# Optimization experiments

Measured on AMD Instinct MI355X. Metric: run time of the kernel, lower is better.

Reference implementation:

```python
import jax, jax.numpy as jnp
import numpy as np

OUT_F, IN_F = 4096, 4096
N_FREQ = 10000
SCALING = 150.0


def iwht(x):
    """Unnormalized fast Walsh-Hadamard transform along axis 0. x: [n, m], n power of 2."""
    n, m = x.shape
    steps = int(np.log2(n))
    x = x.reshape((2,) * steps + (m,))
    for ax in range(steps):  # log2(n) butterfly stages
        a, b = jnp.split(x, 2, axis=ax)
        x = jnp.concatenate([a + b, a - b], axis=ax)
    return x.reshape(n, m)


def setup_inputs() -> dict:
    key = jax.random.key(0)
    k1, k2, k3, k4 = jax.random.split(key, 4)
    x = jax.random.normal(k1, (2, 512, IN_F), dtype=jnp.float32)
    weight = jax.random.normal(k2, (OUT_F, IN_F), dtype=jnp.float32) * 0.02
    spectrum = jax.random.normal(k3, (N_FREQ,), dtype=jnp.float32)
    indices = jax.random.randint(k4, (2, N_FREQ), 0, OUT_F, dtype=jnp.int64)
    return {"x": x, "weight": weight, "spectrum": spectrum, "indices": indices}


def reference(x, weight, spectrum, indices):
    out_f, in_f = weight.shape
    # sparse scatter of spectrum into dense (out, in) matrix
    dense = jnp.zeros((out_f, in_f), dtype=spectrum.dtype).at[indices[0], indices[1]].set(spectrum)
    # inverse WHT along out axis, scaled
    delta_w = iwht(dense) * (SCALING / np.sqrt(np.float32(out_f)))
    # F.linear(x, base_w + delta_w)
    return jnp.einsum('bsi,oi->bso', x, weight + delta_w.astype(x.dtype))
```

## Files before the change

### kernel.cpp

```cpp
#include <hip/hip_runtime.h>

typedef unsigned short ushort_t;

#define M_DIM 1024
#define N_DIM 4096
#define K_DIM 4096
#define NFREQ 10000
constexpr float SCALE = 150.0f / 64.0f;

typedef __bf16 bf16x8_t  __attribute__((ext_vector_type(8)));
typedef float  f32x16_t  __attribute__((ext_vector_type(16)));

__device__ inline ushort_t f2bf(float f) {
  union { float f; unsigned u; } v; v.f = f;
  unsigned r = v.u + 0x7fffu + ((v.u >> 16) & 1u);
  return (ushort_t)(r >> 16);
}

__global__ __launch_bounds__(256) void build_w4(
    const float* __restrict__ weight,
    const float* __restrict__ spectrum,
    const int* __restrict__ idx,
    const float* __restrict__ x,
    ushort_t* __restrict__ wb,
    ushort_t* __restrict__ xb) {
  if (blockIdx.y == 16) {
    int flat = blockIdx.x * 256 + threadIdx.x;
#pragma unroll 4
    for (int k = 0; k < 64; ++k) {
      int i = flat + k * 16384;
      float4 v = ((const float4*)x)[i];
      ushort4 o;
      o.x = f2bf(v.x); o.y = f2bf(v.y); o.z = f2bf(v.z); o.w = f2bf(v.w);
      ((ushort4*)xb)[i] = o;
    }
    return;
  }

  constexpr int CAP = 1024;
  __shared__ unsigned e_raw[CAP];
  __shared__ float    v_raw[CAP];
  __shared__ uint2    ev_srt[CAP];
  __shared__ int cnt;
  __shared__ int cstart[65];
  __shared__ int coff[64];
  __shared__ int ccnt[64];
  __shared__ unsigned walsh16[16];

  const int tid = threadIdx.x;
  const int ci0 = blockIdx.x * 64;
  const int o0  = blockIdx.y * 256;

  if (tid == 0) cnt = 0;
  if (tid < 64) ccnt[tid] = 0;
  if (tid < 16) {
    unsigned m = tid;
    unsigned w = (m & 1 ? 0xAAAAu : 0u) ^ (m & 2 ? 0xCCCCu : 0u)
               ^ (m & 4 ? 0xF0F0u : 0u) ^ (m & 8 ? 0xFF00u : 0u);
    walsh16[m] = w;
  }
  __syncthreads();

  for (int j = tid; j < NFREQ; j += 256) {
    int c = idx[NFREQ + j];
    if ((c >> 6) == (int)blockIdx.x) {
      int p = atomicAdd(&cnt, 1);
      if (p < CAP) {
        e_raw[p] = ((unsigned)(c & 63) << 26) | ((unsigned)j << 12) | (unsigned)idx[j];
        v_raw[p] = spectrum[j];
        atomicAdd(&ccnt[c & 63], 1);
      }
    }
  }
  __syncthreads();
  const int n = cnt < CAP ? cnt : CAP;

  if (tid < 64) {
    int v = ccnt[tid];
    int s = v;
    for (int d = 1; d < 64; d <<= 1) {
      int o = __shfl_up(s, d, 64);
      if (tid >= d) s += o;
    }
    cstart[tid + 1] = s;
    if (tid == 0) cstart[0] = 0;
    coff[tid] = s - v;
  }
  __syncthreads();
  for (int e = tid; e < n; e += 256) {
    unsigned w = e_raw[e];
    int dc = w >> 26;
    int p = atomicAdd(&coff[dc], 1);
    ev_srt[p] = make_uint2(w, __float_as_uint(v_raw[e]));
  }
  __syncthreads();

  for (int e = tid; e < n; e += 256) {
    uint2 ev = ev_srt[e];
    int dc = ev.x >> 26;
    unsigned r = ev.x & 0xFFFu, j = (ev.x >> 12) & 0x3FFFu;
    int s0 = cstart[dc], e0 = cstart[dc + 1];
    bool dead = false;
    for (int p = s0; p < e0; ++p) {
      unsigned w2 = ev_srt[p].x;
      if ((w2 & 0xFFFu) == r && ((w2 >> 12) & 0x3FFFu) > j) dead = true;
    }
    if (dead) ev_srt[e].y = 0u;
  }
  __syncthreads();

  const int dc0   = (tid & 15) * 4;
  const int rof   = tid >> 4;
  const int obase = o0 + rof * 16;

  float acc[4][16];
#pragma unroll
  for (int c = 0; c < 4; ++c)
#pragma unroll
    for (int j = 0; j < 16; ++j) acc[c][j] = 0.0f;

#pragma unroll
  for (int c = 0; c < 4; ++c) {
    const int s = cstart[dc0 + c], e = cstart[dc0 + c + 1];
    for (int p = s; p < e; ++p) {
      uint2 ev = ev_srt[p];
      unsigned r = ev.x & 0xFFFu;
      unsigned W = walsh16[r & 15u];
      unsigned sx = ev.y ^ ((unsigned)(__popc(obase & r) & 1) << 31);
#pragma unroll
      for (int j = 0; j < 16; ++j) {
        acc[c][j] += __uint_as_float(sx ^ ((W << (31 - j)) & 0x80000000u));
      }
    }
  }

  size_t g = (size_t)obase * K_DIM + ci0 + dc0;
#pragma unroll
  for (int j = 0; j < 16; ++j) {
    float4 w4 = *(const float4*)&weight[g];
    ushort4 ov;
    ov.x = f2bf(w4.x + SCALE * acc[0][j]);
    ov.y = f2bf(w4.y + SCALE * acc[1][j]);
    ov.z = f2bf(w4.z + SCALE * acc[2][j]);
    ov.w = f2bf(w4.w + SCALE * acc[3][j]);
    *(ushort4*)&wb[g] = ov;
    g += K_DIM;
  }
}

__global__ __launch_bounds__(256) void gemm_bt(
    const ushort_t* __restrict__ A,
    const ushort_t* __restrict__ B,
    float* __restrict__ C0,
    float* __restrict__ C1,
    int klen) {
  constexpr int BM = 128, BN = 128, BK = 64;
  __shared__ __align__(16) ushort_t As[BM * BK];
  __shared__ __align__(16) ushort_t Bs[BN * BK];

  const int tid  = threadIdx.x;
  const int wave = tid >> 6, lane = tid & 63;
  const int wrow = wave >> 1, wcol = wave & 1;
  const int l32  = lane & 31, half = lane >> 5;
  const int bm = blockIdx.y * BM, bn = blockIdx.x * BN;
  const int kbeg = blockIdx.z * klen;
  float* __restrict__ dst = blockIdx.z == 0
      ? C0 : C1 + (size_t)(blockIdx.z - 1) * M_DIM * N_DIM;

  const int srow8 = lane >> 3;
  const int sq    = lane & 7;

  f32x16_t acc[2][2] = {};

  for (int kt = kbeg; kt < kbeg + klen; kt += BK) {
#pragma unroll
    for (int c = 0; c < 4; ++c) {
      int ch = wave * 4 + c;
      int gr = ch * 8 + srow8;
      int qg = sq ^ (gr & 7);
      const ushort_t* ga = A + (size_t)(bm + gr) * K_DIM + kt + qg * 8;
      __builtin_amdgcn_global_load_lds(
          (const __attribute__((address_space(1))) void*)ga,
          (__attribute__((address_space(3))) void*)&As[ch * 512], 16, 0, 0);
      const ushort_t* gb = B + (size_t)(bn + gr) * K_DIM + kt + qg * 8;
      __builtin_amdgcn_global_load_lds(
          (const __attribute__((address_space(1))) void*)gb,
          (__attribute__((address_space(3))) void*)&Bs[ch * 512], 16, 0, 0);
    }
    __syncthreads();

    bf16x8_t af[2][4], bfr[2][4];
#pragma unroll
    for (int mi = 0; mi < 2; ++mi) {
#pragma unroll
      for (int h = 0; h < 4; ++h) {
        int q = h * 2 + half;
        int ar = wrow * 64 + mi * 32 + l32;
        af[mi][h]  = *(const bf16x8_t*)&As[ar * BK + ((q ^ (ar & 7)) * 8)];
        int br = wcol * 64 + mi * 32 + l32;
        bfr[mi][h] = *(const bf16x8_t*)&Bs[br * BK + ((q ^ (br & 7)) * 8)];
      }
    }
#pragma unroll
    for (int h = 0; h < 4; ++h)
#pragma unroll
      for (int mi = 0; mi < 2; ++mi)
#pragma unroll
        for (int nj = 0; nj < 2; ++nj)
          acc[mi][nj] = __builtin_amdgcn_mfma_f32_32x32x16_bf16(
              af[mi][h], bfr[nj][h], acc[mi][nj], 0, 0, 0);
    __syncthreads();
  }

#pragma unroll
  for (int mi = 0; mi < 2; ++mi) {
#pragma unroll
    for (int nj = 0; nj < 2; ++nj) {
      int col  = bn + wcol * 64 + nj * 32 + l32;
      int rwb  = bm + wrow * 64 + mi * 32 + 4 * half;
#pragma unroll
      for (int reg = 0; reg < 16; ++reg) {
        int row = rwb + (reg & 3) + 8 * (reg >> 2);
        dst[(size_t)row * N_DIM + col] = acc[mi][nj][reg];
      }
    }
  }
}

__global__ __launch_bounds__(256) void reduce_n(float* __restrict__ out,
                                                const float* __restrict__ part,
                                                int npart) {
  int i = blockIdx.x * 256 + threadIdx.x;
  float4 a = ((const float4*)out)[i];
  for (int t = 0; t < npart; ++t) {
    float4 b = ((const float4*)(part + (size_t)t * M_DIM * N_DIM))[i];
    a.x += b.x; a.y += b.y; a.z += b.z; a.w += b.w;
  }
  ((float4*)out)[i] = a;
}

extern "C" void kernel_launch(void* const* d_in, const int* in_sizes, int n_in,
                              void* d_out, int out_size, void* d_ws, size_t ws_size,
                              hipStream_t stream) {
  const float* x        = (const float*)d_in[0];
  const float* weight   = (const float*)d_in[1];
  const float* spectrum = (const float*)d_in[2];
  const int*   indices  = (const int*)d_in[3];
  float* out = (float*)d_out;

  char* ws = (char*)d_ws;
  const size_t WB_BYTES = (size_t)N_DIM * K_DIM * 2;
  const size_t XB_BYTES = (size_t)M_DIM * K_DIM * 2;
  const size_t P1_BYTES = (size_t)M_DIM * N_DIM * 4;

  ushort_t* wb = (ushort_t*)ws;
  ushort_t* xb = (ushort_t*)(ws + WB_BYTES);
  float* part = (float*)(ws + WB_BYTES + XB_BYTES);

  int zsplit = (ws_size >= WB_BYTES + XB_BYTES + P1_BYTES) ? 2 : 1;

  build_w4<<<dim3(64, 17), 256, 0, stream>>>(weight, spectrum, indices, x, wb, xb);

  gemm_bt<<<dim3(N_DIM / 128, M_DIM / 128, zsplit), 256, 0, stream>>>(
      xb, wb, out, part, K_DIM / zsplit);
  if (zsplit > 1)
    reduce_n<<<(M_DIM * N_DIM / 4) / 256, 256, 0, stream>>>(out, part, zsplit - 1);
}
```

Measured before the change: 185.5 us.

## Hoist sparse entry sorting into prep kernel and allow 4-way split-K

The per-column-group gather, counting sort and duplicate resolution of the sparse spectrum entries moves out of the weight-build kernel into a separate 64-block prep kernel. Its results are written to workspace, so each of the 16 row blocks per column group only loads them instead of redoing the 10000-index scan. The scratch area for these entries aliases the split-K partial buffer, which the GEMM only writes after the build kernel has consumed the entries. The GEMM split-K factor also rises to 4 when the workspace allows it. That gives more blocks in flight, but the final reduction must read three partial buffers and the launch sequence gains one extra kernel.

```diff
diff --git a/kernel.cpp b/kernel.cpp
--- a/kernel.cpp
+++ b/kernel.cpp
@@ -17,11 +17,84 @@
   return (ushort_t)(r >> 16);
 }
 
-__global__ __launch_bounds__(256) void build_w4(
-    const float* __restrict__ weight,
+__global__ __launch_bounds__(256) void prep_entries(
     const float* __restrict__ spectrum,
     const int* __restrict__ idx,
+    uint2* __restrict__ ent,
+    int* __restrict__ cst) {
+  constexpr int CAP = 1024;
+  __shared__ unsigned e_raw[CAP];
+  __shared__ float    v_raw[CAP];
+  __shared__ uint2    ev_srt[CAP];
+  __shared__ int cnt;
+  __shared__ int cstart[65];
+  __shared__ int coff[64];
+  __shared__ int ccnt[64];
+
+  const int tid = threadIdx.x;
+  const int g = blockIdx.x;
+
+  if (tid == 0) cnt = 0;
+  if (tid < 64) ccnt[tid] = 0;
+  __syncthreads();
+
+  for (int j = tid; j < NFREQ; j += 256) {
+    int c = idx[NFREQ + j];
+    if ((c >> 6) == g) {
+      int p = atomicAdd(&cnt, 1);
+      if (p < CAP) {
+        e_raw[p] = ((unsigned)(c & 63) << 26) | ((unsigned)j << 12) | (unsigned)idx[j];
+        v_raw[p] = spectrum[j];
+        atomicAdd(&ccnt[c & 63], 1);
+      }
+    }
+  }
+  __syncthreads();
+  const int n = cnt < CAP ? cnt : CAP;
+
+  if (tid < 64) {
+    int v = ccnt[tid];
+    int s = v;
+    for (int d = 1; d < 64; d <<= 1) {
+      int o = __shfl_up(s, d, 64);
+      if (tid >= d) s += o;
+    }
+    cstart[tid + 1] = s;
+    if (tid == 0) cstart[0] = 0;
+    coff[tid] = s - v;
+  }
+  __syncthreads();
+  for (int e = tid; e < n; e += 256) {
+    unsigned w = e_raw[e];
+    int dc = w >> 26;
+    int p = atomicAdd(&coff[dc], 1);
+    ev_srt[p] = make_uint2(w, __float_as_uint(v_raw[e]));
+  }
+  __syncthreads();
+
+  for (int e = tid; e < n; e += 256) {
+    uint2 ev = ev_srt[e];
+    int dc = ev.x >> 26;
+    unsigned r = ev.x & 0xFFFu, j = (ev.x >> 12) & 0x3FFFu;
+    int s0 = cstart[dc], e0 = cstart[dc + 1];
+    bool dead = false;
+    for (int p = s0; p < e0; ++p) {
+      unsigned w2 = ev_srt[p].x;
+      if ((w2 & 0xFFFu) == r && ((w2 >> 12) & 0x3FFFu) > j) dead = true;
+    }
+    if (dead) ev_srt[e].y = 0u;
+  }
+  __syncthreads();
+
+  for (int e = tid; e < n; e += 256) ent[g * CAP + e] = ev_srt[e];
+  if (tid < 65) cst[g * 72 + tid] = cstart[tid];
+}
+
+__global__ __launch_bounds__(256) void apply_w(
+    const float* __restrict__ weight,
     const float* __restrict__ x,
+    const uint2* __restrict__ ent,
+    const int* __restrict__ cst,
     ushort_t* __restrict__ wb,
     ushort_t* __restrict__ xb) {
   if (blockIdx.y == 16) {
@@ -38,75 +111,24 @@
   }
 
   constexpr int CAP = 1024;
-  __shared__ unsigned e_raw[CAP];
-  __shared__ float    v_raw[CAP];
-  __shared__ uint2    ev_srt[CAP];
-  __shared__ int cnt;
+  __shared__ uint2 ev[CAP];
   __shared__ int cstart[65];
-  __shared__ int coff[64];
-  __shared__ int ccnt[64];
   __shared__ unsigned walsh16[16];
 
   const int tid = threadIdx.x;
-  const int ci0 = blockIdx.x * 64;
+  const int g   = blockIdx.x;
+  const int ci0 = g * 64;
   const int o0  = blockIdx.y * 256;
 
-  if (tid == 0) cnt = 0;
-  if (tid < 64) ccnt[tid] = 0;
+  const int n = cst[g * 72 + 64];
+  if (tid < 65) cstart[tid] = cst[g * 72 + tid];
   if (tid < 16) {
     unsigned m = tid;
     unsigned w = (m & 1 ? 0xAAAAu : 0u) ^ (m & 2 ? 0xCCCCu : 0u)
                ^ (m & 4 ? 0xF0F0u : 0u) ^ (m & 8 ? 0xFF00u : 0u);
     walsh16[m] = w;
   }
-  __syncthreads();
-
-  for (int j = tid; j < NFREQ; j += 256) {
-    int c = idx[NFREQ + j];
-    if ((c >> 6) == (int)blockIdx.x) {
-      int p = atomicAdd(&cnt, 1);
-      if (p < CAP) {
-        e_raw[p] = ((unsigned)(c & 63) << 26) | ((unsigned)j << 12) | (unsigned)idx[j];
-        v_raw[p] = spectrum[j];
-        atomicAdd(&ccnt[c & 63], 1);
-      }
-    }
-  }
-  __syncthreads();
-  const int n = cnt < CAP ? cnt : CAP;
-
-  if (tid < 64) {
-    int v = ccnt[tid];
-    int s = v;
-    for (int d = 1; d < 64; d <<= 1) {
-      int o = __shfl_up(s, d, 64);
-      if (tid >= d) s += o;
-    }
-    cstart[tid + 1] = s;
-    if (tid == 0) cstart[0] = 0;
-    coff[tid] = s - v;
-  }
-  __syncthreads();
-  for (int e = tid; e < n; e += 256) {
-    unsigned w = e_raw[e];
-    int dc = w >> 26;
-    int p = atomicAdd(&coff[dc], 1);
-    ev_srt[p] = make_uint2(w, __float_as_uint(v_raw[e]));
-  }
-  __syncthreads();
-
-  for (int e = tid; e < n; e += 256) {
-    uint2 ev = ev_srt[e];
-    int dc = ev.x >> 26;
-    unsigned r = ev.x & 0xFFFu, j = (ev.x >> 12) & 0x3FFFu;
-    int s0 = cstart[dc], e0 = cstart[dc + 1];
-    bool dead = false;
-    for (int p = s0; p < e0; ++p) {
-      unsigned w2 = ev_srt[p].x;
-      if ((w2 & 0xFFFu) == r && ((w2 >> 12) & 0x3FFFu) > j) dead = true;
-    }
-    if (dead) ev_srt[e].y = 0u;
-  }
+  for (int e = tid; e < n; e += 256) ev[e] = ent[g * CAP + e];
   __syncthreads();
 
   const int dc0   = (tid & 15) * 4;
@@ -123,10 +145,10 @@
   for (int c = 0; c < 4; ++c) {
     const int s = cstart[dc0 + c], e = cstart[dc0 + c + 1];
     for (int p = s; p < e; ++p) {
-      uint2 ev = ev_srt[p];
-      unsigned r = ev.x & 0xFFFu;
+      uint2 evv = ev[p];
+      unsigned r = evv.x & 0xFFFu;
       unsigned W = walsh16[r & 15u];
-      unsigned sx = ev.y ^ ((unsigned)(__popc(obase & r) & 1) << 31);
+      unsigned sx = evv.y ^ ((unsigned)(__popc(obase & r) & 1) << 31);
 #pragma unroll
       for (int j = 0; j < 16; ++j) {
         acc[c][j] += __uint_as_float(sx ^ ((W << (31 - j)) & 0x80000000u));
@@ -134,17 +156,17 @@
     }
   }
 
-  size_t g = (size_t)obase * K_DIM + ci0 + dc0;
+  size_t gaddr = (size_t)obase * K_DIM + ci0 + dc0;
 #pragma unroll
   for (int j = 0; j < 16; ++j) {
-    float4 w4 = *(const float4*)&weight[g];
+    float4 w4 = *(const float4*)&weight[gaddr];
     ushort4 ov;
     ov.x = f2bf(w4.x + SCALE * acc[0][j]);
     ov.y = f2bf(w4.y + SCALE * acc[1][j]);
     ov.z = f2bf(w4.z + SCALE * acc[2][j]);
     ov.w = f2bf(w4.w + SCALE * acc[3][j]);
-    *(ushort4*)&wb[g] = ov;
-    g += K_DIM;
+    *(ushort4*)&wb[gaddr] = ov;
+    gaddr += K_DIM;
   }
 }
 
@@ -249,17 +271,23 @@
   float* out = (float*)d_out;
 
   char* ws = (char*)d_ws;
-  const size_t WB_BYTES = (size_t)N_DIM * K_DIM * 2;
-  const size_t XB_BYTES = (size_t)M_DIM * K_DIM * 2;
-  const size_t P1_BYTES = (size_t)M_DIM * N_DIM * 4;
+  const size_t WB_BYTES  = (size_t)N_DIM * K_DIM * 2;
+  const size_t XB_BYTES  = (size_t)M_DIM * K_DIM * 2;
+  const size_t P1_BYTES  = (size_t)M_DIM * N_DIM * 4;
+  const size_t ENT_BYTES = (size_t)64 * 1024 * sizeof(uint2);
 
   ushort_t* wb = (ushort_t*)ws;
   ushort_t* xb = (ushort_t*)(ws + WB_BYTES);
-  float* part = (float*)(ws + WB_BYTES + XB_BYTES);
-
-  int zsplit = (ws_size >= WB_BYTES + XB_BYTES + P1_BYTES) ? 2 : 1;
-
-  build_w4<<<dim3(64, 17), 256, 0, stream>>>(weight, spectrum, indices, x, wb, xb);
+  char* scratch = ws + WB_BYTES + XB_BYTES;
+  uint2* ent = (uint2*)scratch;
+  int*   cst = (int*)(scratch + ENT_BYTES);
+  float* part = (float*)scratch;
+
+  int zsplit = (ws_size >= WB_BYTES + XB_BYTES + 3 * P1_BYTES) ? 4
+             : (ws_size >= WB_BYTES + XB_BYTES + P1_BYTES)     ? 2 : 1;
+
+  prep_entries<<<64, 256, 0, stream>>>(spectrum, indices, ent, cst);
+  apply_w<<<dim3(64, 17), 256, 0, stream>>>(weight, x, ent, cst, wb, xb);
 
   gemm_bt<<<dim3(N_DIM / 128, M_DIM / 128, zsplit), 256, 0, stream>>>(
       xb, wb, out, part, K_DIM / zsplit);
```

After: 201.2 us. 8.5% more time.

## Batch loads in build kernel and remap GEMM tiles per XCD for L2 locality

Applied to the files above, without the earlier changes.

The x-to-bf16 conversion now issues eight independent float4 loads before converting and storing, which raises memory-level parallelism. The weight tile loads in build_w4 are hoisted ahead of the sparse accumulation loop so their latency overlaps the Walsh accumulation, at the cost of 64 extra live registers. The GEMM block index is remapped so that blocks landing on the same XCD (round-robin by flat id mod 8) cover a contiguous 8x4 region of the output tile grid, improving L2 reuse of A and B tiles.

```diff
diff --git a/kernel.cpp b/kernel.cpp
--- a/kernel.cpp
+++ b/kernel.cpp
@@ -26,13 +26,18 @@
     ushort_t* __restrict__ xb) {
   if (blockIdx.y == 16) {
     int flat = blockIdx.x * 256 + threadIdx.x;
-#pragma unroll 4
-    for (int k = 0; k < 64; ++k) {
-      int i = flat + k * 16384;
-      float4 v = ((const float4*)x)[i];
-      ushort4 o;
-      o.x = f2bf(v.x); o.y = f2bf(v.y); o.z = f2bf(v.z); o.w = f2bf(v.w);
-      ((ushort4*)xb)[i] = o;
+    for (int kk = 0; kk < 8; ++kk) {
+      float4 v[8];
+#pragma unroll
+      for (int u = 0; u < 8; ++u)
+        v[u] = ((const float4*)x)[flat + (kk * 8 + u) * 16384];
+#pragma unroll
+      for (int u = 0; u < 8; ++u) {
+        ushort4 o;
+        o.x = f2bf(v[u].x); o.y = f2bf(v[u].y);
+        o.z = f2bf(v[u].z); o.w = f2bf(v[u].w);
+        ((ushort4*)xb)[flat + (kk * 8 + u) * 16384] = o;
+      }
     }
     return;
   }
@@ -113,6 +118,12 @@
   const int rof   = tid >> 4;
   const int obase = o0 + rof * 16;
 
+  const size_t gaddr = (size_t)obase * K_DIM + ci0 + dc0;
+  float4 wv[16];
+#pragma unroll
+  for (int j = 0; j < 16; ++j)
+    wv[j] = *(const float4*)&weight[gaddr + (size_t)j * K_DIM];
+
   float acc[4][16];
 #pragma unroll
   for (int c = 0; c < 4; ++c)
@@ -134,17 +145,14 @@
     }
   }
 
-  size_t g = (size_t)obase * K_DIM + ci0 + dc0;
 #pragma unroll
   for (int j = 0; j < 16; ++j) {
-    float4 w4 = *(const float4*)&weight[g];
     ushort4 ov;
-    ov.x = f2bf(w4.x + SCALE * acc[0][j]);
-    ov.y = f2bf(w4.y + SCALE * acc[1][j]);
-    ov.z = f2bf(w4.z + SCALE * acc[2][j]);
-    ov.w = f2bf(w4.w + SCALE * acc[3][j]);
-    *(ushort4*)&wb[g] = ov;
-    g += K_DIM;
+    ov.x = f2bf(wv[j].x + SCALE * acc[0][j]);
+    ov.y = f2bf(wv[j].y + SCALE * acc[1][j]);
+    ov.z = f2bf(wv[j].z + SCALE * acc[2][j]);
+    ov.w = f2bf(wv[j].w + SCALE * acc[3][j]);
+    *(ushort4*)&wb[gaddr + (size_t)j * K_DIM] = ov;
   }
 }
 
@@ -162,7 +170,14 @@
   const int wave = tid >> 6, lane = tid & 63;
   const int wrow = wave >> 1, wcol = wave & 1;
   const int l32  = lane & 31, half = lane >> 5;
-  const int bm = blockIdx.y * BM, bn = blockIdx.x * BN;
+
+  const int fid = blockIdx.y * 32 + blockIdx.x;
+  const int xcd = fid & 7, w8 = fid >> 3;
+  const int sx = w8 & 7, sy = w8 >> 3;
+  const int cx = xcd & 3, cy = xcd >> 2;
+  const int bn = (cx * 8 + sx) * BN;
+  const int bm = (cy * 4 + sy) * BM;
+
   const int kbeg = blockIdx.z * klen;
   float* __restrict__ dst = blockIdx.z == 0
       ? C0 : C1 + (size_t)(blockIdx.z - 1) * M_DIM * N_DIM;
```

After: 199.9 us. +7.8%, slower.
